# Kernel tuning notes

Hardware: AMD Instinct MI355X
Metric: run time of the kernel (lower is better)

The kernel has to match this reference:

```python
import jax, jax.numpy as jnp
import numpy as np

T, B, D = 512, 64, 1024


def setup_inputs() -> dict:
    key = jax.random.key(0)
    k1, k2, k3, k4, k5 = jax.random.split(key, 5)
    s = 1.0 / np.sqrt(D)  # torch RNNCell init scale
    return {
        "x": jax.random.normal(k1, (T, B, D), dtype=jnp.float32),
        "W_ih": jax.random.normal(k2, (D, D), dtype=jnp.float32) * s,
        "W_hh": jax.random.normal(k3, (D, D), dtype=jnp.float32) * s,
        "b_ih": jax.random.normal(k4, (D,), dtype=jnp.float32) * s,
        "b_hh": jax.random.normal(k5, (D,), dtype=jnp.float32) * s,
    }


def reference(x, W_ih, W_hh, b_ih, b_hh):
    """CustomRNN forward: sequential Elman cell over time-major input.

    x: [T, B, D]; returns (output [T, B, D], final hidden [B, D]).
    """
    # Precompute the input projection for all timesteps in one big GEMM
    # (same math as per-step x_t @ W_ih^T + b_ih, just batched).
    xproj = jnp.einsum("tbd,hd->tbh", x, W_ih) + b_ih  # [T, B, D]

    def step(h, xp_t):
        h_new = jnp.tanh(xp_t + h @ W_hh.T + b_hh)  # [B, D]
        return h_new, h_new

    h0 = jnp.zeros((x.shape[1], W_hh.shape[0]), dtype=x.dtype)
    h_final, output = jax.lax.scan(step, h0, xproj)
    return output, h_final
```

## Files before the change

kernel.cpp:

```cpp
#include <hip/hip_runtime.h>
#include <hip/hip_bf16.h>

#define T_LEN 512
#define B_SZ  64
#define D_SZ  1024

typedef __attribute__((ext_vector_type(8))) short  short8;
typedef __attribute__((ext_vector_type(4))) float  f32x4;
typedef __attribute__((ext_vector_type(4))) unsigned short ushort4v;
typedef __attribute__((ext_vector_type(4))) unsigned int   uint4v;

__device__ __forceinline__ float bf2f(unsigned short u) {
    unsigned int x = ((unsigned int)u) << 16;
    return __uint_as_float(x);
}
__device__ __forceinline__ unsigned short f2bf(float f) {
    unsigned int x = __float_as_uint(f);
    unsigned int r = x + 0x7FFFu + ((x >> 16) & 1u);
    return (unsigned short)(r >> 16);
}
__device__ __forceinline__ void split2p(float f, unsigned short* hi, unsigned short* lo) {
    unsigned short h = f2bf(f);
    *hi = h;
    *lo = f2bf(f - bf2f(h));
}
__device__ __forceinline__ float fast_tanh(float x) {
    float xx = fminf(fmaxf(x, -20.0f), 20.0f);
    float e2 = __expf(2.0f * xx);
    return __fdividef(e2 - 1.0f, e2 + 1.0f);
}

#define CNT_STRIDE 64

__global__ void init_kernel(int* slot) {
    int i = threadIdx.x;
    if (i < 8 * CNT_STRIDE) slot[i] = 0;
}

#define BM 128
#define BN 128
#define BK 32
#define ASTR (BK + 8)

__global__ __launch_bounds__(256) void xproj_kernel(
    const float* __restrict__ x, const float* __restrict__ Wih,
    const float* __restrict__ bih, float* __restrict__ xp)
{
    __shared__ unsigned short Ah[BM][ASTR];
    __shared__ unsigned short Al[BM][ASTR];
    __shared__ unsigned short Bh[BN][ASTR];
    __shared__ unsigned short Bl[BN][ASTR];

    const int nblk = D_SZ / BN;
    const int bm = blockIdx.x / nblk;
    const int bn = blockIdx.x % nblk;
    const int m0 = bm * BM, n0 = bn * BN;
    const int tid  = threadIdx.x;
    const int lane = tid & 63, wave = tid >> 6;
    const int wm = wave >> 1, wn = wave & 1;

    f32x4 acc[4][4];
#pragma unroll
    for (int i = 0; i < 4; i++)
#pragma unroll
        for (int j = 0; j < 4; j++) acc[i][j] = (f32x4)0.0f;

    const int ar = lane & 15;
    const int kb = (lane >> 4) << 3;

    for (int k0 = 0; k0 < D_SZ; k0 += BK) {
#pragma unroll
        for (int i = 0; i < 4; i++) {
            int f4  = tid + i * 256;
            int row = f4 >> 3;
            int c4  = (f4 & 7) << 2;
            f32x4 va = *reinterpret_cast<const f32x4*>(x   + (size_t)(m0 + row) * D_SZ + k0 + c4);
            f32x4 vb = *reinterpret_cast<const f32x4*>(Wih + (size_t)(n0 + row) * D_SZ + k0 + c4);
            ushort4v pah, pal, pbh, pbl;
#pragma unroll
            for (int e = 0; e < 4; e++) {
                unsigned short h_, l_;
                split2p(va[e], &h_, &l_); pah[e] = h_; pal[e] = l_;
                split2p(vb[e], &h_, &l_); pbh[e] = h_; pbl[e] = l_;
            }
            *reinterpret_cast<ushort4v*>(&Ah[row][c4]) = pah;
            *reinterpret_cast<ushort4v*>(&Al[row][c4]) = pal;
            *reinterpret_cast<ushort4v*>(&Bh[row][c4]) = pbh;
            *reinterpret_cast<ushort4v*>(&Bl[row][c4]) = pbl;
        }
        __syncthreads();

        short8 ah[4], al[4], bh[4], bl[4];
#pragma unroll
        for (int mi = 0; mi < 4; mi++) {
            ah[mi] = *reinterpret_cast<const short8*>(&Ah[wm * 64 + mi * 16 + ar][kb]);
            al[mi] = *reinterpret_cast<const short8*>(&Al[wm * 64 + mi * 16 + ar][kb]);
        }
#pragma unroll
        for (int ni = 0; ni < 4; ni++) {
            bh[ni] = *reinterpret_cast<const short8*>(&Bh[wn * 64 + ni * 16 + ar][kb]);
            bl[ni] = *reinterpret_cast<const short8*>(&Bl[wn * 64 + ni * 16 + ar][kb]);
        }
#pragma unroll
        for (int mi = 0; mi < 4; mi++)
#pragma unroll
            for (int ni = 0; ni < 4; ni++) {
                acc[mi][ni] = __builtin_amdgcn_mfma_f32_16x16x32_bf16(ah[mi], bh[ni], acc[mi][ni], 0, 0, 0);
                acc[mi][ni] = __builtin_amdgcn_mfma_f32_16x16x32_bf16(al[mi], bh[ni], acc[mi][ni], 0, 0, 0);
                acc[mi][ni] = __builtin_amdgcn_mfma_f32_16x16x32_bf16(ah[mi], bl[ni], acc[mi][ni], 0, 0, 0);
            }
        __syncthreads();
    }

    const int r0 = (lane >> 4) * 4;
    const int cl = lane & 15;
#pragma unroll
    for (int mi = 0; mi < 4; mi++) {
#pragma unroll
        for (int ni = 0; ni < 4; ni++) {
            int col = n0 + wn * 64 + ni * 16 + cl;
            float bias = bih[col];
            size_t base = (size_t)(m0 + wm * 64 + mi * 16 + r0) * D_SZ + col;
#pragma unroll
            for (int r = 0; r < 4; r++)
                xp[base + (size_t)r * D_SZ] = acc[mi][ni][r] + bias;
        }
    }
}

#define MR 8
#define NC 64
#define HSTR (D_SZ + 8)
#define WSTR 520

__global__ __launch_bounds__(256, 1) void rnn_kernel(
    const float* __restrict__ xp, const float* __restrict__ Whh,
    const float* __restrict__ bhh, float* __restrict__ out,
    unsigned int* hbuf, int* slot)
{
    __shared__ unsigned short Hh[16][HSTR];
    __shared__ unsigned short Hl[16][HSTR];
    __shared__ unsigned short Wlo[4][16][WSTR];

    const int wg = blockIdx.x;
    const int b  = wg & 7;
    const int c  = wg >> 3;
    const int tid  = threadIdx.x;
    const int lane = tid & 63, wave = tid >> 6;

    const int cl   = lane & 15;
    const int hi4  = lane >> 4;
    const int kb   = hi4 << 3;
    const int colg = c * NC + wave * 16 + cl;
    const float bias = bhh[colg];
    const int rloc = hi4 * 4;
    const bool active = (hi4 < 2);

    int* tslot = slot + b * CNT_STRIDE;
    const int myslot = c * 4 + wave;

    short8 wh[32], wl_r[16];
    {
        const float* wrow = Whh + (size_t)colg * D_SZ;
#pragma unroll
        for (int kk = 0; kk < 32; kk++) {
            f32x4 v0 = *reinterpret_cast<const f32x4*>(wrow + kk * 32 + kb);
            f32x4 v1 = *reinterpret_cast<const f32x4*>(wrow + kk * 32 + kb + 4);
            short8 sh, sl;
#pragma unroll
            for (int e = 0; e < 4; e++) {
                unsigned short h_, l_;
                split2p(v0[e], &h_, &l_); sh[e] = (short)h_; sl[e] = (short)l_;
                split2p(v1[e], &h_, &l_); sh[4 + e] = (short)h_; sl[4 + e] = (short)l_;
            }
            wh[kk] = sh;
            if (kk < 16) wl_r[kk] = sl;
            else *reinterpret_cast<short8*>(&Wlo[wave][cl][(kk - 16) * 32 + kb]) = sl;
        }
    }
    for (int i = tid; i < 16 * HSTR; i += 256) {
        (&Hh[0][0])[i] = 0;
        (&Hl[0][0])[i] = 0;
    }
    __syncthreads();

    for (int t = 0; t < T_LEN; t++) {
        float xv[4];
        const float* xpt = xp + ((size_t)t * B_SZ + b * MR) * D_SZ;
        if (active) {
#pragma unroll
            for (int r = 0; r < 4; r++)
                xv[r] = xpt[(size_t)(rloc + r) * D_SZ + colg];
        }

        if (t > 0) {
            for (int tries = 0; tries < 400000; ++tries) {
                int v = __hip_atomic_load(tslot + lane, __ATOMIC_RELAXED, __HIP_MEMORY_SCOPE_AGENT);
                if (__all(v >= t)) break;
            }

            const uint4v* hsrc16 = reinterpret_cast<const uint4v*>(
                hbuf + ((size_t)(t & 1) * B_SZ + b * MR) * D_SZ);
            uint4v vv[8];
#pragma unroll
            for (int i = 0; i < 8; i++)
                asm volatile("global_load_dwordx4 %0, %1, off sc0 sc1"
                             : "=v"(vv[i]) : "v"(hsrc16 + tid + i * 256) : "memory");
            asm volatile("s_waitcnt vmcnt(0)" ::: "memory");
            __builtin_amdgcn_sched_barrier(0);
#pragma unroll
            for (int i = 0; i < 8; i++) {
                int j   = tid + i * 256;
                int row = j >> 8;
                int c4  = (j & 255) << 2;
                ushort4v hh, hl;
#pragma unroll
                for (int e = 0; e < 4; e++) {
                    unsigned int u = vv[i][e];
                    hh[e] = (unsigned short)(u & 0xFFFFu);
                    hl[e] = (unsigned short)(u >> 16);
                }
                *reinterpret_cast<ushort4v*>(&Hh[row][c4]) = hh;
                *reinterpret_cast<ushort4v*>(&Hl[row][c4]) = hl;
            }
            __syncthreads();
        }

        f32x4 a0 = (f32x4)0.0f, a1 = (f32x4)0.0f, a2 = (f32x4)0.0f;
#pragma unroll
        for (int kk = 0; kk < 16; kk++) {
            short8 ah  = *reinterpret_cast<const short8*>(&Hh[cl][kk * 32 + kb]);
            short8 alo = *reinterpret_cast<const short8*>(&Hl[cl][kk * 32 + kb]);
            a0 = __builtin_amdgcn_mfma_f32_16x16x32_bf16(ah,  wh[kk],   a0, 0, 0, 0);
            a1 = __builtin_amdgcn_mfma_f32_16x16x32_bf16(alo, wh[kk],   a1, 0, 0, 0);
            a2 = __builtin_amdgcn_mfma_f32_16x16x32_bf16(ah,  wl_r[kk], a2, 0, 0, 0);
        }
#pragma unroll
        for (int kk = 16; kk < 32; kk++) {
            short8 ah  = *reinterpret_cast<const short8*>(&Hh[cl][kk * 32 + kb]);
            short8 alo = *reinterpret_cast<const short8*>(&Hl[cl][kk * 32 + kb]);
            short8 wlv = *reinterpret_cast<const short8*>(&Wlo[wave][cl][(kk - 16) * 32 + kb]);
            a0 = __builtin_amdgcn_mfma_f32_16x16x32_bf16(ah,  wh[kk], a0, 0, 0, 0);
            a1 = __builtin_amdgcn_mfma_f32_16x16x32_bf16(alo, wh[kk], a1, 0, 0, 0);
            a2 = __builtin_amdgcn_mfma_f32_16x16x32_bf16(ah,  wlv,    a2, 0, 0, 0);
        }

        float hval[4];
        if (active) {
            unsigned int* hdst = hbuf + ((size_t)((t + 1) & 1) * B_SZ + b * MR) * D_SZ;
#pragma unroll
            for (int r = 0; r < 4; r++) {
                int row = rloc + r;
                float pre = (a0[r] + a1[r] + a2[r]) + xv[r] + bias;
                float h = fast_tanh(pre);
                hval[r] = h;
                unsigned short hh_, ll_;
                split2p(h, &hh_, &ll_);
                unsigned int packed = (unsigned int)hh_ | ((unsigned int)ll_ << 16);
                __hip_atomic_store(&hdst[(size_t)row * D_SZ + colg], packed,
                                   __ATOMIC_RELAXED, __HIP_MEMORY_SCOPE_AGENT);
            }
        }
        asm volatile("s_waitcnt vmcnt(0)" ::: "memory");
        if (lane == 0)
            __hip_atomic_store(tslot + myslot, t + 1, __ATOMIC_RELAXED, __HIP_MEMORY_SCOPE_AGENT);

        if (active) {
            float* outt = out + ((size_t)t * B_SZ + b * MR) * D_SZ;
#pragma unroll
            for (int r = 0; r < 4; r++) {
                int row = rloc + r;
                outt[(size_t)row * D_SZ + colg] = hval[r];
                if (t == T_LEN - 1)
                    out[(size_t)T_LEN * B_SZ * D_SZ + (size_t)(b * MR + row) * D_SZ + colg] = hval[r];
            }
        }
    }
}

extern "C" void kernel_launch(void* const* d_in, const int* in_sizes, int n_in,
                              void* d_out, int out_size, void* d_ws, size_t ws_size,
                              hipStream_t stream)
{
    const float* x   = (const float*)d_in[0];
    const float* Wih = (const float*)d_in[1];
    const float* Whh = (const float*)d_in[2];
    const float* bih = (const float*)d_in[3];
    const float* bhh = (const float*)d_in[4];
    float* out = (float*)d_out;

    char* ws = (char*)d_ws;
    float*        xp   = (float*)ws;
    unsigned int* hbuf = (unsigned int*)(ws + 134217728);
    int*          slot = (int*)(ws + 134217728 + 524288);

    init_kernel<<<dim3(1), dim3(512), 0, stream>>>(slot);
    xproj_kernel<<<dim3(2048), dim3(256), 0, stream>>>(x, Wih, bih, xp);
    rnn_kernel<<<dim3(128), dim3(256), 0, stream>>>(xp, Whh, bhh, out, hbuf, slot);
}
```

Before: 2.298 ms.

## Split hidden-state wait and load into two K halves to overlap with MFMA

The per-step wait for all producer slots is split in two. The kernel first waits only for the producers of the first 512 columns (plus its own group), loads that half of h, and runs the first 16 MFMA k-steps. Only then does it wait for the remaining producers and load the second half. This is meant to overlap cross-workgroup synchronisation latency with compute, at the cost of an extra barrier and a second polling loop per step.

```diff
diff --git a/kernel.cpp b/kernel.cpp
--- a/kernel.cpp
+++ b/kernel.cpp
@@ -158,6 +158,7 @@
 
     int* tslot = slot + b * CNT_STRIDE;
     const int myslot = c * 4 + wave;
+    const unsigned long long need1 = 0xFFFFFFFFull | (0xFull << (c * 4));
 
     short8 wh[32], wl_r[16];
     {
@@ -193,26 +194,30 @@
                 xv[r] = xpt[(size_t)(rloc + r) * D_SZ + colg];
         }
 
+        const uint4v* hsrc16 = reinterpret_cast<const uint4v*>(
+            hbuf + ((size_t)(t & 1) * B_SZ + b * MR) * D_SZ);
+
         if (t > 0) {
             for (int tries = 0; tries < 400000; ++tries) {
                 int v = __hip_atomic_load(tslot + lane, __ATOMIC_RELAXED, __HIP_MEMORY_SCOPE_AGENT);
-                if (__all(v >= t)) break;
-            }
-
-            const uint4v* hsrc16 = reinterpret_cast<const uint4v*>(
-                hbuf + ((size_t)(t & 1) * B_SZ + b * MR) * D_SZ);
-            uint4v vv[8];
-#pragma unroll
-            for (int i = 0; i < 8; i++)
+                unsigned long long rdy = __ballot(v >= t);
+                if ((rdy & need1) == need1) break;
+            }
+            uint4v vv[4];
+#pragma unroll
+            for (int i = 0; i < 4; i++) {
+                int jh = tid + i * 256;
+                int ti = ((jh >> 7) << 8) + (jh & 127);
                 asm volatile("global_load_dwordx4 %0, %1, off sc0 sc1"
-                             : "=v"(vv[i]) : "v"(hsrc16 + tid + i * 256) : "memory");
+                             : "=v"(vv[i]) : "v"(hsrc16 + ti) : "memory");
+            }
             asm volatile("s_waitcnt vmcnt(0)" ::: "memory");
             __builtin_amdgcn_sched_barrier(0);
 #pragma unroll
-            for (int i = 0; i < 8; i++) {
-                int j   = tid + i * 256;
-                int row = j >> 8;
-                int c4  = (j & 255) << 2;
+            for (int i = 0; i < 4; i++) {
+                int jh  = tid + i * 256;
+                int row = jh >> 7;
+                int c4  = (jh & 127) << 2;
                 ushort4v hh, hl;
 #pragma unroll
                 for (int e = 0; e < 4; e++) {
@@ -235,6 +240,41 @@
             a1 = __builtin_amdgcn_mfma_f32_16x16x32_bf16(alo, wh[kk],   a1, 0, 0, 0);
             a2 = __builtin_amdgcn_mfma_f32_16x16x32_bf16(ah,  wl_r[kk], a2, 0, 0, 0);
         }
+
+        if (t > 0) {
+            for (int tries = 0; tries < 400000; ++tries) {
+                int v = __hip_atomic_load(tslot + lane, __ATOMIC_RELAXED, __HIP_MEMORY_SCOPE_AGENT);
+                unsigned long long rdy = __ballot(v >= t);
+                if (rdy == ~0ull) break;
+            }
+            uint4v vv[4];
+#pragma unroll
+            for (int i = 0; i < 4; i++) {
+                int jh = tid + i * 256;
+                int ti = ((jh >> 7) << 8) + 128 + (jh & 127);
+                asm volatile("global_load_dwordx4 %0, %1, off sc0 sc1"
+                             : "=v"(vv[i]) : "v"(hsrc16 + ti) : "memory");
+            }
+            asm volatile("s_waitcnt vmcnt(0)" ::: "memory");
+            __builtin_amdgcn_sched_barrier(0);
+#pragma unroll
+            for (int i = 0; i < 4; i++) {
+                int jh  = tid + i * 256;
+                int row = jh >> 7;
+                int c4  = 512 + ((jh & 127) << 2);
+                ushort4v hh, hl;
+#pragma unroll
+                for (int e = 0; e < 4; e++) {
+                    unsigned int u = vv[i][e];
+                    hh[e] = (unsigned short)(u & 0xFFFFu);
+                    hl[e] = (unsigned short)(u >> 16);
+                }
+                *reinterpret_cast<ushort4v*>(&Hh[row][c4]) = hh;
+                *reinterpret_cast<ushort4v*>(&Hl[row][c4]) = hl;
+            }
+            __syncthreads();
+        }
+
 #pragma unroll
         for (int kk = 16; kk < 32; kk++) {
             short8 ah  = *reinterpret_cast<const short8*>(&Hh[cl][kk * 32 + kb]);
```

Result: slower. 2.495 ms (+8.5%).
